# Kernel tuning notes

Measured on AMD Instinct MI355X. Metric: run time of the kernel, lower is better.

Reference implementation:

```python
import jax, jax.numpy as jnp
import numpy as np

N = 100000
E = 1600000
IN = 256
H = 4
C = 64


def setup_inputs() -> dict:
    key = jax.random.key(0)
    k1, k2, k3, k4, k5, k6 = jax.random.split(key, 6)
    x = jax.random.normal(k1, (N, IN), dtype=jnp.float32)
    edge_index = jax.random.randint(k2, (2, E), 0, N, dtype=jnp.int64)
    W = jax.random.normal(k3, (IN, H * C), dtype=jnp.float32) * (1.0 / np.sqrt(IN))
    att_src = jax.random.normal(k4, (H, C), dtype=jnp.float32) * 0.1
    att_dst = jax.random.normal(k5, (H, C), dtype=jnp.float32) * 0.1
    bias = jax.random.normal(k6, (H * C,), dtype=jnp.float32) * 0.01
    return {"x": x, "edge_index": edge_index, "W": W, "att_src": att_src, "att_dst": att_dst, "bias": bias}


def reference(x, edge_index, W, att_src, att_dst, bias):
    n = x.shape[0]
    # PyG GATConv default: add self-loops
    loops = jnp.arange(n, dtype=edge_index.dtype)
    src = jnp.concatenate([edge_index[0], loops])  # [E+N]
    dst = jnp.concatenate([edge_index[1], loops])  # [E+N]
    xp = (x @ W).reshape(n, H, C)                   # [N,H,C]
    a_src = jnp.einsum('nhc,hc->nh', xp, att_src)   # [N,H]
    a_dst = jnp.einsum('nhc,hc->nh', xp, att_dst)   # [N,H]
    # per-edge attention logits, LeakyReLU(0.2)
    alpha = jax.nn.leaky_relu(a_src[src] + a_dst[dst], negative_slope=0.2)  # [E+N,H]
    # segment softmax over destination neighborhoods (every node has a self-loop)
    amax = jax.ops.segment_max(alpha, dst, num_segments=n)
    amax = jnp.where(jnp.isfinite(amax), amax, 0.0)
    ex = jnp.exp(alpha - amax[dst])
    denom = jax.ops.segment_sum(ex, dst, num_segments=n)
    w = ex / denom[dst]                              # [E+N,H]
    # weighted scatter-add of source features
    msg = xp[src] * w[..., None]                     # [E+N,H,C]
    agg = jax.ops.segment_sum(msg, dst, num_segments=n)  # [N,H,C]
    out = agg.reshape(n, H * C) + bias
    return jax.nn.elu(out)
```

## Files before the change

kernel.cpp:

```cpp
#include <hip/hip_runtime.h>
#include <hip/hip_fp16.h>

#define FDIM 256
#define NH 4

typedef float f32x4 __attribute__((ext_vector_type(4)));
typedef int   i32x4 __attribute__((ext_vector_type(4)));
typedef short short8v __attribute__((ext_vector_type(8)));
typedef unsigned short ushort_t;
typedef unsigned short ushort8 __attribute__((ext_vector_type(8)));

__device__ __forceinline__ float leaky02(float v) { return v > 0.0f ? v : 0.2f * v; }

__device__ __forceinline__ ushort_t f2bf(float f) {
    union { float f; unsigned int u; } v; v.f = f;
    unsigned int u = v.u + 0x7FFFu + ((v.u >> 16) & 1u);
    return (ushort_t)(u >> 16);
}

__device__ __forceinline__ float bf2f(ushort_t u) {
    union { float f; unsigned int u; } v;
    v.u = ((unsigned int)u) << 16;
    return v.f;
}

__device__ __forceinline__ void gload_lds16(const void* g, void* lds) {
    __builtin_amdgcn_global_load_lds((const __attribute__((address_space(1))) unsigned int*)g,
                                     (__attribute__((address_space(3))) unsigned int*)lds, 16, 0, 0);
}

__device__ __forceinline__ float recw(const i32x4& r, int h) {
    unsigned v = (h < 2) ? (unsigned)r.y : (unsigned)r.z;
    unsigned bits = (h & 1) ? (v >> 16) : (v & 0xFFFFu);
    __half_raw hr; hr.x = (unsigned short)bits;
    return __half2float(*reinterpret_cast<__half*>(&hr));
}

__global__ __launch_bounds__(256) void wprep_kernel(const float* __restrict__ W,
                                                    ushort_t* __restrict__ Wbf) {
    const int k = blockIdx.x;
    const int col = threadIdx.x;
    Wbf[(((size_t)(k >> 3) * 256 + col) << 3) + (k & 7)] = f2bf(W[(size_t)k * 256 + col]);
}

__global__ __launch_bounds__(512) void gemm_xp_kernel(const float* __restrict__ x,
                                                      const ushort_t* __restrict__ Wbf,
                                                      const float* __restrict__ att_s,
                                                      const float* __restrict__ att_d,
                                                      ushort_t* __restrict__ xpb,
                                                      float* __restrict__ a_src,
                                                      float* __restrict__ a_dst, int n,
                                                      const int* __restrict__ dst,
                                                      int* __restrict__ counts,
                                                      ushort_t* __restrict__ rank, int E) {
    __shared__ ushort_t a_lds[4096];
    __shared__ ushort_t b_lds[8192];
    const int t = threadIdx.x;

    {
        const int per = (E + gridDim.x - 1) / gridDim.x;
        const int lo = blockIdx.x * per;
        const int hi = min(lo + per, E);
        for (int e = lo + t; e < hi; e += 512) {
            const int d = __builtin_nontemporal_load(&dst[e]);
            rank[e] = (ushort_t)atomicAdd(&counts[d], 1);
        }
    }

    const int w = t >> 6, l = t & 63;
    const int wm = w >> 2, wn = w & 3;
    const int row0 = blockIdx.x << 7;
    const int fr = l & 15, fk = l >> 4;

    const int arow = t & 127, akb = t >> 7;
    int grow = row0 + arow;
    if (grow >= n) grow = n - 1;
    const float* aptr = x + (size_t)grow * FDIM + (akb << 3);

    f32x4 acc[4][4] = {};

    for (int s = 0; s < 8; ++s) {
        float4 v0 = *(const float4*)(aptr + s * 32);
        float4 v1 = *(const float4*)(aptr + s * 32 + 4);
        ushort8 u;
        u[0]=f2bf(v0.x); u[1]=f2bf(v0.y); u[2]=f2bf(v0.z); u[3]=f2bf(v0.w);
        u[4]=f2bf(v1.x); u[5]=f2bf(v1.y); u[6]=f2bf(v1.z); u[7]=f2bf(v1.w);

        if (s) __syncthreads();

        *(ushort8*)&a_lds[(((size_t)akb << 7) + arow) << 3] = u;
        gload_lds16(Wbf + (size_t)s * 8192 + ((size_t)t << 3), (char*)b_lds + (w << 10));
        gload_lds16(Wbf + (size_t)s * 8192 + ((size_t)(t + 512) << 3), (char*)b_lds + 8192 + (w << 10));
        __syncthreads();

        short8v af[4], bfv[4];
        #pragma unroll
        for (int m = 0; m < 4; ++m)
            af[m] = *(const short8v*)&a_lds[(((size_t)fk << 7) + wm * 64 + m * 16 + fr) << 3];
        #pragma unroll
        for (int nf = 0; nf < 4; ++nf)
            bfv[nf] = *(const short8v*)&b_lds[(((size_t)fk << 8) + wn * 64 + nf * 16 + fr) << 3];
        #pragma unroll
        for (int m = 0; m < 4; ++m)
            #pragma unroll
            for (int nf = 0; nf < 4; ++nf)
                acc[m][nf] = __builtin_amdgcn_mfma_f32_16x16x32_bf16(af[m], bfv[nf], acc[m][nf], 0, 0, 0);
    }

    #pragma unroll
    for (int m = 0; m < 4; ++m) {
        const int r_ = row0 + wm * 64 + m * 16 + fk * 4;
        #pragma unroll
        for (int nf = 0; nf < 4; ++nf) {
            const int c_ = wn * 64 + nf * 16 + fr;
            #pragma unroll
            for (int j = 0; j < 4; ++j)
                if (r_ + j < n)
                    xpb[(size_t)(r_ + j) * FDIM + c_] = f2bf(acc[m][nf][j]);
        }
    }

    float att_sv[4], att_dv[4];
    #pragma unroll
    for (int nf = 0; nf < 4; ++nf) {
        att_sv[nf] = att_s[(wn << 6) + (nf << 4) + fr];
        att_dv[nf] = att_d[(wn << 6) + (nf << 4) + fr];
    }
    #pragma unroll
    for (int m = 0; m < 4; ++m) {
        #pragma unroll
        for (int j = 0; j < 4; ++j) {
            float ps = acc[m][0][j] * att_sv[0] + acc[m][1][j] * att_sv[1]
                     + acc[m][2][j] * att_sv[2] + acc[m][3][j] * att_sv[3];
            float pd = acc[m][0][j] * att_dv[0] + acc[m][1][j] * att_dv[1]
                     + acc[m][2][j] * att_dv[2] + acc[m][3][j] * att_dv[3];
            ps += __shfl_xor(ps, 1, 64); pd += __shfl_xor(pd, 1, 64);
            ps += __shfl_xor(ps, 2, 64); pd += __shfl_xor(pd, 2, 64);
            ps += __shfl_xor(ps, 4, 64); pd += __shfl_xor(pd, 4, 64);
            ps += __shfl_xor(ps, 8, 64); pd += __shfl_xor(pd, 8, 64);
            if (fr == 0) {
                const int r_ = row0 + wm * 64 + m * 16 + fk * 4 + j;
                if (r_ < n) {
                    a_src[r_ * NH + wn] = ps;
                    a_dst[r_ * NH + wn] = pd;
                }
            }
        }
    }
}

__global__ __launch_bounds__(256) void scan_partial_kernel(const int* __restrict__ counts,
                                                           int* __restrict__ blockSums, int n) {
    __shared__ int sdata[256];
    const int b = blockIdx.x, t = threadIdx.x;
    const int base = b * 1024 + t * 4;
    int s = 0;
    #pragma unroll
    for (int j = 0; j < 4; ++j)
        if (base + j < n) s += counts[base + j];
    sdata[t] = s;
    __syncthreads();
    for (int off = 128; off > 0; off >>= 1) {
        if (t < off) sdata[t] += sdata[t + off];
        __syncthreads();
    }
    if (t == 0) blockSums[b] = sdata[0];
}

__global__ __launch_bounds__(256) void scan_final_kernel(const int* __restrict__ counts,
                                                         const int* __restrict__ blockSums,
                                                         int* __restrict__ offsets, int n, int nb) {
    __shared__ int s[256];
    __shared__ int bs[256];
    const int b = blockIdx.x, t = threadIdx.x;
    int bv = (t < nb) ? blockSums[t] : 0;
    bs[t] = bv;
    __syncthreads();
    for (int d = 1; d < 256; d <<= 1) {
        int u = (t >= d) ? bs[t - d] : 0;
        __syncthreads();
        bs[t] += u;
        __syncthreads();
    }
    const int blockOff = (b > 0) ? bs[b - 1] : 0;

    const int base = b * 1024 + t * 4;
    int c[4];
    int tsum = 0;
    #pragma unroll
    for (int j = 0; j < 4; ++j) {
        c[j] = (base + j < n) ? counts[base + j] : 0;
        tsum += c[j];
    }
    s[t] = tsum;
    __syncthreads();
    for (int d = 1; d < 256; d <<= 1) {
        int u = (t >= d) ? s[t - d] : 0;
        __syncthreads();
        s[t] += u;
        __syncthreads();
    }
    int run = s[t] - tsum + blockOff;
    #pragma unroll
    for (int j = 0; j < 4; ++j) {
        if (base + j < n) {
            offsets[base + j] = run;
            run += c[j];
        }
    }
}

__global__ void scatter_kernel(const int* __restrict__ src, const int* __restrict__ dst,
                               const ushort_t* __restrict__ rank,
                               const float* __restrict__ a_src, const float* __restrict__ a_dst,
                               const int* __restrict__ offsets,
                               i32x4* __restrict__ erec, int E) {
    int stride = gridDim.x * blockDim.x;
    for (int e = blockIdx.x * blockDim.x + threadIdx.x; e < E; e += stride) {
        const int s = __builtin_nontemporal_load(&src[e]);
        const int d = __builtin_nontemporal_load(&dst[e]);
        const int r = rank[e];
        const float4 as = ((const float4*)a_src)[s];
        const float4 ad = ((const float4*)a_dst)[d];
        const float w0 = __expf(leaky02(as.x + ad.x));
        const float w1 = __expf(leaky02(as.y + ad.y));
        const float w2 = __expf(leaky02(as.z + ad.z));
        const float w3 = __expf(leaky02(as.w + ad.w));
        union { __half2 h; int i; } p01, p23;
        p01.h = __floats2half2_rn(w0, w1);
        p23.h = __floats2half2_rn(w2, w3);
        i32x4 rec;
        rec.x = s; rec.y = p01.i; rec.z = p23.i; rec.w = 0;
        const int pos = offsets[d] + r;
        __builtin_nontemporal_store(rec, &erec[pos]);
    }
}

__global__ __launch_bounds__(256) void aggregate_kernel(const ushort_t* __restrict__ xpb,
                                                        const float* __restrict__ a_src,
                                                        const float* __restrict__ a_dst,
                                                        const int* __restrict__ offsets,
                                                        const int* __restrict__ counts,
                                                        const i32x4* __restrict__ erec,
                                                        const float* __restrict__ bias,
                                                        float* __restrict__ out, int n) {
    const int i = (blockIdx.x << 2) + (threadIdx.x >> 6);
    if (i >= n) return;
    const int lane = threadIdx.x & 63;
    const int halfid = lane >> 5, sl = lane & 31;
    const int h = sl >> 3;
    const size_t colb = (size_t)sl << 3;
    const int start = offsets[i];
    const int cnt = counts[i];
    const i32x4* recs = erec + start;

    float acc[8] = {};
    float den = 0.f;

    int e = 0;
    for (; e + 4 <= cnt; e += 4) {
        const i32x4 ra = recs[e + halfid];
        const i32x4 rb = recs[e + 2 + halfid];
        const ushort8 ua = *(const ushort8*)(xpb + (size_t)ra.x * FDIM + colb);
        const ushort8 ub = *(const ushort8*)(xpb + (size_t)rb.x * FDIM + colb);
        const float wa = recw(ra, h), wb = recw(rb, h);
        den += wa + wb;
        #pragma unroll
        for (int j = 0; j < 8; ++j) acc[j] = fmaf(wa, bf2f(ua[j]), acc[j]);
        #pragma unroll
        for (int j = 0; j < 8; ++j) acc[j] = fmaf(wb, bf2f(ub[j]), acc[j]);
    }
    for (; e < cnt; e += 2) {
        const int idx = e + halfid;
        const int cidx = idx < cnt ? idx : cnt - 1;
        const i32x4 r = recs[cidx];
        const ushort8 u = *(const ushort8*)(xpb + (size_t)r.x * FDIM + colb);
        const float wv = idx < cnt ? recw(r, h) : 0.f;
        den += wv;
        #pragma unroll
        for (int j = 0; j < 8; ++j) acc[j] = fmaf(wv, bf2f(u[j]), acc[j]);
    }
    if (halfid == 0) {
        const float ws = __expf(leaky02(a_src[i * NH + h] + a_dst[i * NH + h]));
        const ushort8 u = *(const ushort8*)(xpb + (size_t)i * FDIM + colb);
        den += ws;
        #pragma unroll
        for (int j = 0; j < 8; ++j) acc[j] = fmaf(ws, bf2f(u[j]), acc[j]);
    }
    den += __shfl_xor(den, 32, 64);
    #pragma unroll
    for (int j = 0; j < 8; ++j) acc[j] += __shfl_xor(acc[j], 32, 64);

    const float inv = 1.0f / den;
    const int c0 = (sl << 3) + (halfid << 2);
    const float4 b4 = *(const float4*)(bias + c0);
    const int jb = halfid << 2;
    f32x4 v;
    v.x = acc[jb + 0] * inv + b4.x;
    v.y = acc[jb + 1] * inv + b4.y;
    v.z = acc[jb + 2] * inv + b4.z;
    v.w = acc[jb + 3] * inv + b4.w;
    v.x = v.x > 0.f ? v.x : (__expf(v.x) - 1.f);
    v.y = v.y > 0.f ? v.y : (__expf(v.y) - 1.f);
    v.z = v.z > 0.f ? v.z : (__expf(v.z) - 1.f);
    v.w = v.w > 0.f ? v.w : (__expf(v.w) - 1.f);
    *(f32x4*)(out + (size_t)i * FDIM + c0) = v;
}

extern "C" void kernel_launch(void* const* d_in, const int* in_sizes, int n_in,
                              void* d_out, int out_size, void* d_ws, size_t ws_size,
                              hipStream_t stream) {
    const float* x       = (const float*)d_in[0];
    const int*   ei      = (const int*)d_in[1];
    const float* W       = (const float*)d_in[2];
    const float* att_s   = (const float*)d_in[3];
    const float* att_d   = (const float*)d_in[4];
    const float* bias    = (const float*)d_in[5];
    float* out = (float*)d_out;

    const int n = in_sizes[0] / FDIM;
    const int E = in_sizes[1] / 2;
    const int* src = ei;
    const int* dst = ei + E;

    char* ws = (char*)d_ws;
    size_t off = 0;
    auto alloc = [&](size_t bytes) -> void* {
        void* p = ws + off;
        off = (off + bytes + 255) & ~(size_t)255;
        return p;
    };
    ushort_t* xpb  = (ushort_t*)alloc((size_t)n * FDIM * sizeof(ushort_t));
    float* a_src   = (float*)alloc((size_t)n * NH * sizeof(float));
    float* a_dst   = (float*)alloc((size_t)n * NH * sizeof(float));
    int* counts    = (int*)alloc((size_t)n * sizeof(int));
    int* offsets   = (int*)alloc((size_t)n * sizeof(int));
    int* blockSums = (int*)alloc(256 * sizeof(int));
    ushort_t* rank = (ushort_t*)alloc((size_t)E * sizeof(ushort_t));
    i32x4* erec    = (i32x4*)alloc((size_t)E * sizeof(i32x4));
    ushort_t* Wbf  = (ushort_t*)alloc((size_t)FDIM * FDIM * sizeof(ushort_t));
    (void)ws_size;

    hipMemsetAsync(counts, 0, (size_t)n * sizeof(int), stream);

    wprep_kernel<<<256, 256, 0, stream>>>(W, Wbf);
    gemm_xp_kernel<<<(n + 127) / 128, 512, 0, stream>>>(x, Wbf, att_s, att_d, xpb, a_src, a_dst, n,
                                                        dst, counts, rank, E);
    const int nb = (n + 1023) / 1024;
    scan_partial_kernel<<<nb, 256, 0, stream>>>(counts, blockSums, n);
    scan_final_kernel<<<nb, 256, 0, stream>>>(counts, blockSums, offsets, n, nb);
    scatter_kernel<<<2048, 256, 0, stream>>>(src, dst, rank, a_src, a_dst, offsets, erec, E);
    aggregate_kernel<<<(n + 3) / 4, 256, 0, stream>>>(xpb, a_src, a_dst, offsets, counts, erec,
                                                      bias, out, n);
}
```

Before: 320.5 us.

## Load GEMM fragments directly from global memory and split histogram into own kernel

The x@W GEMM no longer stages A and B tiles through LDS with barriers. Each wave now loads its bf16 fragments directly from global memory into registers and prefetches the next K step. The destination histogram/rank atomics move from the GEMM prologue into a separate grid-stride kernel. This removes LDS traffic and synchronisation, but each A row is now loaded by several waves, and the histogram no longer overlaps with GEMM work.

```diff
diff --git a/kernel.cpp b/kernel.cpp
--- a/kernel.cpp
+++ b/kernel.cpp
@@ -24,11 +24,6 @@
     return v.f;
 }
 
-__device__ __forceinline__ void gload_lds16(const void* g, void* lds) {
-    __builtin_amdgcn_global_load_lds((const __attribute__((address_space(1))) unsigned int*)g,
-                                     (__attribute__((address_space(3))) unsigned int*)lds, 16, 0, 0);
-}
-
 __device__ __forceinline__ float recw(const i32x4& r, int h) {
     unsigned v = (h < 2) ? (unsigned)r.y : (unsigned)r.z;
     unsigned bits = (h & 1) ? (v >> 16) : (v & 0xFFFFu);
@@ -41,6 +36,16 @@
     const int k = blockIdx.x;
     const int col = threadIdx.x;
     Wbf[(((size_t)(k >> 3) * 256 + col) << 3) + (k & 7)] = f2bf(W[(size_t)k * 256 + col]);
+}
+
+__global__ __launch_bounds__(256) void hist_kernel(const int* __restrict__ dst,
+                                                   int* __restrict__ counts,
+                                                   ushort_t* __restrict__ rank, int E) {
+    int stride = gridDim.x * blockDim.x;
+    for (int e = blockIdx.x * blockDim.x + threadIdx.x; e < E; e += stride) {
+        const int d = __builtin_nontemporal_load(&dst[e]);
+        rank[e] = (ushort_t)atomicAdd(&counts[d], 1);
+    }
 }
 
 __global__ __launch_bounds__(512) void gemm_xp_kernel(const float* __restrict__ x,
@@ -49,62 +54,66 @@
                                                       const float* __restrict__ att_d,
                                                       ushort_t* __restrict__ xpb,
                                                       float* __restrict__ a_src,
-                                                      float* __restrict__ a_dst, int n,
-                                                      const int* __restrict__ dst,
-                                                      int* __restrict__ counts,
-                                                      ushort_t* __restrict__ rank, int E) {
-    __shared__ ushort_t a_lds[4096];
-    __shared__ ushort_t b_lds[8192];
+                                                      float* __restrict__ a_dst, int n) {
     const int t = threadIdx.x;
-
-    {
-        const int per = (E + gridDim.x - 1) / gridDim.x;
-        const int lo = blockIdx.x * per;
-        const int hi = min(lo + per, E);
-        for (int e = lo + t; e < hi; e += 512) {
-            const int d = __builtin_nontemporal_load(&dst[e]);
-            rank[e] = (ushort_t)atomicAdd(&counts[d], 1);
-        }
-    }
-
     const int w = t >> 6, l = t & 63;
     const int wm = w >> 2, wn = w & 3;
     const int row0 = blockIdx.x << 7;
     const int fr = l & 15, fk = l >> 4;
 
-    const int arow = t & 127, akb = t >> 7;
-    int grow = row0 + arow;
-    if (grow >= n) grow = n - 1;
-    const float* aptr = x + (size_t)grow * FDIM + (akb << 3);
+    const float* arow_p[4];
+    #pragma unroll
+    for (int m = 0; m < 4; ++m) {
+        int row = row0 + wm * 64 + m * 16 + fr;
+        if (row >= n) row = n - 1;
+        arow_p[m] = x + (size_t)row * FDIM + (fk << 3);
+    }
+    const ushort_t* bcol_p = Wbf + (((size_t)fk << 8) + wn * 64 + fr) * 8;
+
+    float4 a0[4], a1[4], na0[4], na1[4];
+    short8v bf_[4], nbf[4];
+
+    #pragma unroll
+    for (int m = 0; m < 4; ++m) {
+        a0[m] = *(const float4*)(arow_p[m]);
+        a1[m] = *(const float4*)(arow_p[m] + 4);
+    }
+    #pragma unroll
+    for (int nf = 0; nf < 4; ++nf)
+        bf_[nf] = *(const short8v*)(bcol_p + nf * 128);
 
     f32x4 acc[4][4] = {};
 
     for (int s = 0; s < 8; ++s) {
-        float4 v0 = *(const float4*)(aptr + s * 32);
-        float4 v1 = *(const float4*)(aptr + s * 32 + 4);
-        ushort8 u;
-        u[0]=f2bf(v0.x); u[1]=f2bf(v0.y); u[2]=f2bf(v0.z); u[3]=f2bf(v0.w);
-        u[4]=f2bf(v1.x); u[5]=f2bf(v1.y); u[6]=f2bf(v1.z); u[7]=f2bf(v1.w);
-
-        if (s) __syncthreads();
-
-        *(ushort8*)&a_lds[(((size_t)akb << 7) + arow) << 3] = u;
-        gload_lds16(Wbf + (size_t)s * 8192 + ((size_t)t << 3), (char*)b_lds + (w << 10));
-        gload_lds16(Wbf + (size_t)s * 8192 + ((size_t)(t + 512) << 3), (char*)b_lds + 8192 + (w << 10));
-        __syncthreads();
-
-        short8v af[4], bfv[4];
+        if (s < 7) {
+            #pragma unroll
+            for (int m = 0; m < 4; ++m) {
+                na0[m] = *(const float4*)(arow_p[m] + (s + 1) * 32);
+                na1[m] = *(const float4*)(arow_p[m] + (s + 1) * 32 + 4);
+            }
+            #pragma unroll
+            for (int nf = 0; nf < 4; ++nf)
+                nbf[nf] = *(const short8v*)(bcol_p + (size_t)(s + 1) * 8192 + nf * 128);
+        }
+        short8v af[4];
+        #pragma unroll
+        for (int m = 0; m < 4; ++m) {
+            ushort8 u;
+            u[0]=f2bf(a0[m].x); u[1]=f2bf(a0[m].y); u[2]=f2bf(a0[m].z); u[3]=f2bf(a0[m].w);
+            u[4]=f2bf(a1[m].x); u[5]=f2bf(a1[m].y); u[6]=f2bf(a1[m].z); u[7]=f2bf(a1[m].w);
+            af[m] = *(short8v*)&u;
+        }
         #pragma unroll
         for (int m = 0; m < 4; ++m)
-            af[m] = *(const short8v*)&a_lds[(((size_t)fk << 7) + wm * 64 + m * 16 + fr) << 3];
-        #pragma unroll
-        for (int nf = 0; nf < 4; ++nf)
-            bfv[nf] = *(const short8v*)&b_lds[(((size_t)fk << 8) + wn * 64 + nf * 16 + fr) << 3];
-        #pragma unroll
-        for (int m = 0; m < 4; ++m)
             #pragma unroll
             for (int nf = 0; nf < 4; ++nf)
-                acc[m][nf] = __builtin_amdgcn_mfma_f32_16x16x32_bf16(af[m], bfv[nf], acc[m][nf], 0, 0, 0);
+                acc[m][nf] = __builtin_amdgcn_mfma_f32_16x16x32_bf16(af[m], bf_[nf], acc[m][nf], 0, 0, 0);
+        if (s < 7) {
+            #pragma unroll
+            for (int m = 0; m < 4; ++m) { a0[m] = na0[m]; a1[m] = na1[m]; }
+            #pragma unroll
+            for (int nf = 0; nf < 4; ++nf) bf_[nf] = nbf[nf];
+        }
     }
 
     #pragma unroll
@@ -344,8 +353,8 @@
     hipMemsetAsync(counts, 0, (size_t)n * sizeof(int), stream);
 
     wprep_kernel<<<256, 256, 0, stream>>>(W, Wbf);
-    gemm_xp_kernel<<<(n + 127) / 128, 512, 0, stream>>>(x, Wbf, att_s, att_d, xpb, a_src, a_dst, n,
-                                                        dst, counts, rank, E);
+    hist_kernel<<<2048, 256, 0, stream>>>(dst, counts, rank, E);
+    gemm_xp_kernel<<<(n + 127) / 128, 512, 0, stream>>>(x, Wbf, att_s, att_d, xpb, a_src, a_dst, n);
     const int nb = (n + 1023) / 1024;
     scan_partial_kernel<<<nb, 256, 0, stream>>>(counts, blockSums, n);
     scan_final_kernel<<<nb, 256, 0, stream>>>(counts, blockSums, offsets, n, nb);
```

After: 365.5 us. +14.0%, slower.
